# Performance work log

Hardware: AMD Instinct MI355X
Metric: run time of the kernel (lower is better)

The kernel has to match this reference:

```python
import jax, jax.numpy as jnp
import numpy as np

D_MODEL = 1024
H = 16
D_HEAD = 64  # d_q = d_k = d_v
B = 2
S = 2048


def setup_inputs() -> dict:
    key = jax.random.key(0)
    ks = jax.random.split(key, 12)
    scale = 1.0 / np.sqrt(D_MODEL)
    inp = {
        "q": jax.random.normal(ks[0], (B, S, D_MODEL), dtype=jnp.float32),
        "k": jax.random.normal(ks[1], (B, S, D_MODEL), dtype=jnp.float32),
        "v": jax.random.normal(ks[2], (B, S, D_MODEL), dtype=jnp.float32),
        "mask": jax.random.uniform(ks[3], (S, S), dtype=jnp.float32),
        # stacked per-head projection weights: [H, d_model, d_head]
        "W_q": jax.random.normal(ks[4], (H, D_MODEL, D_HEAD), dtype=jnp.float32) * scale,
        "b_q": jnp.zeros((H, D_HEAD), dtype=jnp.float32),
        "W_k": jax.random.normal(ks[5], (H, D_MODEL, D_HEAD), dtype=jnp.float32) * scale,
        "b_k": jnp.zeros((H, D_HEAD), dtype=jnp.float32),
        "W_v": jax.random.normal(ks[6], (H, D_MODEL, D_HEAD), dtype=jnp.float32) * scale,
        "b_v": jnp.zeros((H, D_HEAD), dtype=jnp.float32),
        # output projection: [H*d_v, d_model]
        "W_o": jax.random.normal(ks[7], (H * D_HEAD, D_MODEL), dtype=jnp.float32) * (1.0 / np.sqrt(H * D_HEAD)),
        "b_o": jnp.zeros((D_MODEL,), dtype=jnp.float32),
    }
    return inp


def reference(q, k, v, mask, W_q, b_q, W_k, b_k, W_v, b_v, W_o, b_o):
    # Batched QKV projections over all heads (original loops per head).
    Q = jnp.einsum("bsd,hde->bhse", q, W_q) + b_q[None, :, None, :]  # [B,H,S,Dh]
    K = jnp.einsum("bsd,hde->bhse", k, W_k) + b_k[None, :, None, :]
    V = jnp.einsum("bsd,hde->bhse", v, W_v) + b_v[None, :, None, :]
    scale = 1.0 / jnp.sqrt(jnp.asarray(D_HEAD, dtype=Q.dtype))
    # NOTE: mask is MULTIPLICATIVE on the scaled scores (as in the original).
    scores = jnp.einsum("bhse,bhte->bhst", Q, K) * scale * mask  # [B,H,S,S]
    attn = jax.nn.softmax(scores, axis=-1)
    heads = jnp.einsum("bhst,bhte->bhse", attn, V)  # [B,H,S,Dh]
    # concat heads along feature dim (head order matches torch cat order)
    concat = jnp.transpose(heads, (0, 2, 1, 3)).reshape(B, S, H * D_HEAD)
    return concat @ W_o + b_o
```

## Files before the change

kernel.cpp:

```cpp
#include <hip/hip_runtime.h>
#include <stdint.h>

#define DM 1024
#define HNUM 16
#define DH 64
#define BB 2
#define SSEQ 2048

typedef unsigned short ushort_t;
typedef __attribute__((ext_vector_type(8))) short bf16x8;
typedef __attribute__((ext_vector_type(4))) float f32x4;
typedef __attribute__((ext_vector_type(16))) float f32x16;

#define SCALE2 0.18033688011112042f
#define DEFER_THR 11.0f

__device__ __forceinline__ ushort_t f2bf(float f) {
  unsigned u = __builtin_bit_cast(unsigned, f);
  u += 0x7FFFu + ((u >> 16) & 1u);
  return (ushort_t)(u >> 16);
}
__device__ __forceinline__ float bf2f(ushort_t h) {
  return __builtin_bit_cast(float, (unsigned)h << 16);
}
__device__ __forceinline__ float fast_exp2(float x) {
#if __has_builtin(__builtin_amdgcn_exp2f)
  return __builtin_amdgcn_exp2f(x);
#else
  return exp2f(x);
#endif
}
__device__ __forceinline__ unsigned cvt_pk_bf16(float lo, float hi) {
  unsigned r;
  asm("v_cvt_pk_bf16_f32 %0, %1, %2" : "=v"(r) : "v"(lo), "v"(hi));
  return r;
}
__device__ __forceinline__ void plane32_swap(unsigned& a, unsigned& b, int hh) {
#if __has_builtin(__builtin_amdgcn_permlane32_swap)
  typedef int v2i __attribute__((ext_vector_type(2)));
  v2i r = __builtin_amdgcn_permlane32_swap((int)a, (int)b, 0, 0);
  a = (unsigned)r.x; b = (unsigned)r.y;
#else
  unsigned sa = (unsigned)__shfl_xor((int)a, 32);
  unsigned sb = (unsigned)__shfl_xor((int)b, 32);
  unsigned na = hh ? sb : a;
  unsigned nb = hh ? b : sa;
  a = na; b = nb;
#endif
}

typedef const __attribute__((address_space(1))) unsigned int* gas_ptr;
typedef __attribute__((address_space(3))) unsigned int* las_ptr;
__device__ __forceinline__ void gload_lds16(const void* g, void* l) {
  __builtin_amdgcn_global_load_lds((gas_ptr)(uintptr_t)g, (las_ptr)(uintptr_t)l, 16, 0, 0);
}

__global__ void prep_all(const float* __restrict__ q, const float* __restrict__ k,
                         const float* __restrict__ v, const float* __restrict__ mask,
                         const float* __restrict__ Wq, const float* __restrict__ Wk,
                         const float* __restrict__ Wv, const float* __restrict__ Wo,
                         ushort_t* __restrict__ qd, ushort_t* __restrict__ kd,
                         ushort_t* __restrict__ vd, ushort_t* __restrict__ maskd,
                         ushort_t* __restrict__ dq, ushort_t* __restrict__ dk,
                         ushort_t* __restrict__ dv, ushort_t* __restrict__ dWo) {
  __shared__ ushort_t T[64][65];
  const int bx = blockIdx.x, tid = threadIdx.x;
  if (bx < 6144) {
    const int z = bx >> 11, bi = bx & 2047;
    const float* src = z == 0 ? q : (z == 1 ? k : v);
    ushort_t* dst    = z == 0 ? qd : (z == 1 ? kd : vd);
    const int idx = bi * 256 + tid;
    const float4* s4 = (const float4*)src;
    float4 a = s4[idx * 2], c = s4[idx * 2 + 1];
    union { ushort_t h[8]; uint4 u; } o;
    o.h[0] = f2bf(a.x); o.h[1] = f2bf(a.y); o.h[2] = f2bf(a.z); o.h[3] = f2bf(a.w);
    o.h[4] = f2bf(c.x); o.h[5] = f2bf(c.y); o.h[6] = f2bf(c.z); o.h[7] = f2bf(c.w);
    ((uint4*)dst)[idx] = o.u;
  } else if (bx < 8192) {
    const int TG = bx - 6144;
    const int Tt = TG >> 6, G = TG & 63;
    #pragma unroll
    for (int i = 0; i < 2; ++i) {
      const int wd = tid * 2 + i;
      const int l = wd & 63, g2 = (wd >> 6) & 3, a = wd >> 8;
      const int qr = G * 32 + (l & 31);
      const int t = Tt * 64 + a * 32 + g2 * 8 + (l >> 5) * 4;
      float4 mv = *(const float4*)(mask + (size_t)qr * 2048 + t);
      union { ushort_t h4[4]; uint2 u; } pk;
      pk.h4[0] = f2bf(mv.x * SCALE2); pk.h4[1] = f2bf(mv.y * SCALE2);
      pk.h4[2] = f2bf(mv.z * SCALE2); pk.h4[3] = f2bf(mv.w * SCALE2);
      *(uint2*)(maskd + (size_t)TG * 2048 + (size_t)wd * 4) = pk.u;
    }
  } else if (bx < 8960) {
    const int id = bx - 8192;
    const int zz = id >> 4, yy = id & 15;
    const int mat = zz >> 4, g = zz & 15;
    const float* src = (mat == 0 ? Wq : (mat == 1 ? Wk : Wv)) + (size_t)g * 1024 * 64;
    ushort_t* dst    = (mat == 0 ? dq : (mat == 1 ? dk : dv)) + (size_t)g * 1024 * 64;
    const int r0 = yy * 64;
    #pragma unroll
    for (int i = 0; i < 16; ++i) {
      int idx = i * 256 + tid;
      int r = idx >> 6, c = idx & 63;
      T[r][c] = f2bf(src[(size_t)(r0 + r) * 64 + c]);
    }
    __syncthreads();
    #pragma unroll
    for (int i = 0; i < 16; ++i) {
      int idx = i * 256 + tid;
      int cc = idx >> 6, rr = idx & 63;
      dst[(size_t)cc * 1024 + r0 + rr] = T[rr][cc];
    }
  } else {
    const int id = bx - 8960;
    const int c0 = (id & 15) * 64, r0 = (id >> 4) * 64;
    #pragma unroll
    for (int i = 0; i < 16; ++i) {
      int idx = i * 256 + tid;
      int r = idx >> 6, c = idx & 63;
      T[r][c] = f2bf(Wo[(size_t)(r0 + r) * 1024 + c0 + c]);
    }
    __syncthreads();
    #pragma unroll
    for (int i = 0; i < 16; ++i) {
      int idx = i * 256 + tid;
      int cc = idx >> 6, rr = idx & 63;
      dWo[(size_t)(c0 + cc) * 1024 + r0 + rr] = T[rr][cc];
    }
  }
}

__device__ __forceinline__ void gemm_mainloop_128(const ushort_t* __restrict__ A,
                                                  const ushort_t* __restrict__ Bm,
                                                  f32x4 (&acc)[4][4], int m0, int n0, int l, int w) {
  __shared__ ushort_t As[128 * 64];
  __shared__ ushort_t Bs[128 * 64];
  const int wr = w >> 1, wc = w & 1;
  for (int ks = 0; ks < 16; ++ks) {
    const int k0 = ks * 64;
    #pragma unroll
    for (int it = 0; it < 4; ++it) {
      const int chunk = it * 4 + w;
      const int row = chunk * 8 + (l >> 3);
      const int kc = ((l & 7) * 8) ^ ((row & 7) * 8);
      gload_lds16(A + (size_t)(m0 + row) * 1024 + k0 + kc, (char*)As + chunk * 1024);
      gload_lds16(Bm + (size_t)(n0 + row) * 1024 + k0 + kc, (char*)Bs + chunk * 1024);
    }
    __syncthreads();
    #pragma unroll
    for (int kk = 0; kk < 2; ++kk) {
      bf16x8 af[4], bfr[4];
      #pragma unroll
      for (int mi = 0; mi < 4; ++mi) {
        const int row = wr * 64 + mi * 16 + (l & 15);
        const int kc = (kk * 32 + (l >> 4) * 8) ^ ((row & 7) * 8);
        af[mi] = *(const bf16x8*)(As + row * 64 + kc);
      }
      #pragma unroll
      for (int ni = 0; ni < 4; ++ni) {
        const int row = wc * 64 + ni * 16 + (l & 15);
        const int kc = (kk * 32 + (l >> 4) * 8) ^ ((row & 7) * 8);
        bfr[ni] = *(const bf16x8*)(Bs + row * 64 + kc);
      }
      #pragma unroll
      for (int mi = 0; mi < 4; ++mi)
        #pragma unroll
        for (int ni = 0; ni < 4; ++ni)
          acc[mi][ni] = __builtin_amdgcn_mfma_f32_16x16x32_bf16(af[mi], bfr[ni], acc[mi][ni], 0, 0, 0);
    }
    __syncthreads();
  }
}

__global__ __launch_bounds__(256, 2) void qkv_gemm(
    const ushort_t* __restrict__ qb, const ushort_t* __restrict__ kb, const ushort_t* __restrict__ vb,
    const ushort_t* __restrict__ Wtq, const ushort_t* __restrict__ Wtk, const ushort_t* __restrict__ Wtv,
    const float* __restrict__ bq, const float* __restrict__ bk, const float* __restrict__ bv,
    ushort_t* __restrict__ Qo, ushort_t* __restrict__ Ko, ushort_t* __restrict__ Vto) {
  const int z = blockIdx.z;
  const ushort_t* A  = z == 0 ? qb : (z == 1 ? kb : vb);
  const ushort_t* Bm = z == 0 ? Wtq : (z == 1 ? Wtk : Wtv);
  const float* bias  = z == 0 ? bq : (z == 1 ? bk : bv);
  ushort_t* out      = z == 0 ? Qo : (z == 1 ? Ko : Vto);
  const int m0 = blockIdx.x * 128, n0 = blockIdx.y * 128;
  const int tid = threadIdx.x, l = tid & 63, w = tid >> 6;
  f32x4 acc[4][4] = {};
  gemm_mainloop_128(A, Bm, acc, m0, n0, l, w);
  const int wr = w >> 1, wc = w & 1;
  #pragma unroll
  for (int mi = 0; mi < 4; ++mi) {
    #pragma unroll
    for (int ni = 0; ni < 4; ++ni) {
      const int n = n0 + wc * 64 + ni * 16 + (l & 15);
      const float bb = bias[n];
      const int mbase = m0 + wr * 64 + mi * 16 + ((l >> 4) << 2);
      if (z < 2) {
        #pragma unroll
        for (int i = 0; i < 4; ++i) {
          const int m = mbase + i;
          const size_t o = (((size_t)((m >> 11) * 16 + (n >> 6))) * 2048 + (m & 2047)) * 64 + (n & 63);
          out[o] = f2bf(acc[mi][ni][i] + bb);
        }
      } else {
        union { ushort_t h[4]; uint2 u2; } pk;
        #pragma unroll
        for (int i = 0; i < 4; ++i) pk.h[i] = f2bf(acc[mi][ni][i] + bb);
        const size_t o = (((size_t)((mbase >> 11) * 16 + (n >> 6))) * 64 + (n & 63)) * 2048 + (mbase & 2047);
        *(uint2*)(out + o) = pk.u2;
      }
    }
  }
}

__global__ __launch_bounds__(256, 2) void out_gemm(const ushort_t* __restrict__ A,
                                                   const ushort_t* __restrict__ Bm,
                                                   const float* __restrict__ bias,
                                                   float* __restrict__ out) {
  __shared__ ushort_t As[64 * 64];
  __shared__ ushort_t Bs[128 * 64];
  const int m0 = blockIdx.x * 64, n0 = blockIdx.y * 128;
  const int tid = threadIdx.x, l = tid & 63, w = tid >> 6;
  const int wr = w >> 1, wc = w & 1;
  f32x4 acc[2][4] = {};
  for (int ks = 0; ks < 16; ++ks) {
    const int k0 = ks * 64;
    #pragma unroll
    for (int it = 0; it < 6; ++it) {
      const int chunk = it * 4 + w;
      if (chunk < 8) {
        const int row = chunk * 8 + (l >> 3);
        const int kc = ((l & 7) * 8) ^ ((row & 7) * 8);
        gload_lds16(A + (size_t)(m0 + row) * 1024 + k0 + kc, (char*)As + chunk * 1024);
      } else {
        const int c2 = chunk - 8;
        const int row = c2 * 8 + (l >> 3);
        const int kc = ((l & 7) * 8) ^ ((row & 7) * 8);
        gload_lds16(Bm + (size_t)(n0 + row) * 1024 + k0 + kc, (char*)Bs + c2 * 1024);
      }
    }
    __syncthreads();
    #pragma unroll
    for (int kk = 0; kk < 2; ++kk) {
      bf16x8 af[2], bfr[4];
      #pragma unroll
      for (int mi = 0; mi < 2; ++mi) {
        const int row = wr * 32 + mi * 16 + (l & 15);
        const int kc = (kk * 32 + (l >> 4) * 8) ^ ((row & 7) * 8);
        af[mi] = *(const bf16x8*)(As + row * 64 + kc);
      }
      #pragma unroll
      for (int ni = 0; ni < 4; ++ni) {
        const int row = wc * 64 + ni * 16 + (l & 15);
        const int kc = (kk * 32 + (l >> 4) * 8) ^ ((row & 7) * 8);
        bfr[ni] = *(const bf16x8*)(Bs + row * 64 + kc);
      }
      #pragma unroll
      for (int mi = 0; mi < 2; ++mi)
        #pragma unroll
        for (int ni = 0; ni < 4; ++ni)
          acc[mi][ni] = __builtin_amdgcn_mfma_f32_16x16x32_bf16(af[mi], bfr[ni], acc[mi][ni], 0, 0, 0);
    }
    __syncthreads();
  }
  #pragma unroll
  for (int mi = 0; mi < 2; ++mi) {
    #pragma unroll
    for (int ni = 0; ni < 4; ++ni) {
      const int n = n0 + wc * 64 + ni * 16 + (l & 15);
      const float bb = bias[n];
      const int mbase = m0 + wr * 32 + mi * 16 + ((l >> 4) << 2);
      #pragma unroll
      for (int i = 0; i < 4; ++i)
        out[(size_t)(mbase + i) * 1024 + n] = acc[mi][ni][i] + bb;
    }
  }
}

__device__ __forceinline__ void stage_kv(const ushort_t* __restrict__ Kb, const ushort_t* __restrict__ Vb,
                                         int t0, ushort_t* ks, ushort_t* vs, int l, int w) {
  #pragma unroll
  for (int half = 0; half < 2; ++half) {
    const int c = half * 4 + w;
    const int r1 = c * 8 + (l >> 3);
    const int cc = ((l & 7) * 8) ^ ((r1 & 7) * 8);
    gload_lds16(Kb + (size_t)(t0 + r1) * 64 + cc, (char*)ks + c * 1024);
    gload_lds16(Vb + (size_t)r1 * 2048 + t0 + cc, (char*)vs + c * 1024);
  }
}

__global__ __launch_bounds__(256, 4) void flash_attn(const ushort_t* __restrict__ Q,
                                                     const ushort_t* __restrict__ K,
                                                     const ushort_t* __restrict__ Vt,
                                                     const ushort_t* __restrict__ maskF,
                                                     ushort_t* __restrict__ part0,
                                                     ushort_t* __restrict__ part1,
                                                     float2* __restrict__ mlp) {
  const int bh = blockIdx.y, b = bh >> 4, h = bh & 15;
  const int h2 = blockIdx.z;
  const int tid = threadIdx.x, l = tid & 63, w = tid >> 6;
  const int hh = l >> 5, q_l = l & 31;
  __shared__ ushort_t Ks[2][64 * 64];
  __shared__ ushort_t Vs[2][64 * 64];
  const ushort_t* Qb = Q + (size_t)bh * 2048 * 64;
  const ushort_t* Kb = K + (size_t)bh * 2048 * 64;
  const ushort_t* Vb = Vt + (size_t)bh * 64 * 2048;
  const int qbase = blockIdx.x * 128 + w * 32;
  const int G = qbase >> 5;
  const int tbase = h2 * 1024;

  bf16x8 qf[4];
  #pragma unroll
  for (int s = 0; s < 4; ++s)
    qf[s] = *(const bf16x8*)(Qb + (size_t)(qbase + q_l) * 64 + s * 16 + hh * 8);

  float m_run = -1e30f, l_run = 0.f;
  f32x16 po[2] = {};

  stage_kv(Kb, Vb, tbase, Ks[0], Vs[0], l, w);
  int cur = 0;

  for (int tt = 0; tt < 16; ++tt) {
    const int t0 = tbase + tt * 64;
    __syncthreads();
    if (tt + 1 < 16) stage_kv(Kb, Vb, t0 + 64, Ks[cur ^ 1], Vs[cur ^ 1], l, w);

    const ushort_t* mbase = maskF + (size_t)((t0 >> 6) * 64 + G) * 2048;
    uint2 mw[2][4];
    #pragma unroll
    for (int a = 0; a < 2; ++a)
      #pragma unroll
      for (int g2 = 0; g2 < 4; ++g2)
        mw[a][g2] = *(const uint2*)(mbase + (size_t)(((a * 4 + g2) * 64) + l) * 4);

    f32x16 sc[2] = {};
    #pragma unroll
    for (int s = 0; s < 4; ++s) {
      #pragma unroll
      for (int mt = 0; mt < 2; ++mt) {
        const int row = mt * 32 + q_l;
        const int col = (s * 16 + hh * 8) ^ ((q_l & 7) * 8);
        const bf16x8 kf = *(const bf16x8*)(Ks[cur] + row * 64 + col);
        sc[mt] = __builtin_amdgcn_mfma_f32_32x32x16_bf16(kf, qf[s], sc[mt], 0, 0, 0);
      }
    }

    float tmax = -1e30f;
    #pragma unroll
    for (int a = 0; a < 2; ++a) {
      #pragma unroll
      for (int g2 = 0; g2 < 4; ++g2) {
        const unsigned lo = mw[a][g2].x, hi = mw[a][g2].y;
        float v0 = sc[a][g2 * 4 + 0] * bf2f((ushort_t)lo);
        float v1 = sc[a][g2 * 4 + 1] * bf2f((ushort_t)(lo >> 16));
        float v2 = sc[a][g2 * 4 + 2] * bf2f((ushort_t)hi);
        float v3 = sc[a][g2 * 4 + 3] * bf2f((ushort_t)(hi >> 16));
        sc[a][g2 * 4 + 0] = v0; sc[a][g2 * 4 + 1] = v1;
        sc[a][g2 * 4 + 2] = v2; sc[a][g2 * 4 + 3] = v3;
        tmax = fmaxf(tmax, fmaxf(fmaxf(v0, v1), fmaxf(v2, v3)));
      }
    }
    tmax = fmaxf(tmax, __shfl_xor(tmax, 32));

    if (!__all(tmax <= m_run + DEFER_THR)) {
      const float mnew = fmaxf(m_run, tmax);
      const float rf = fast_exp2(m_run - mnew);
      m_run = mnew;
      l_run *= rf;
      #pragma unroll
      for (int et = 0; et < 2; ++et)
        #pragma unroll
        for (int r = 0; r < 16; ++r) po[et][r] *= rf;
    }

    float psum = 0.f;
    unsigned pw[2][8];
    #pragma unroll
    for (int a = 0; a < 2; ++a)
      #pragma unroll
      for (int j = 0; j < 8; ++j) {
        const float p0 = fast_exp2(sc[a][2 * j] - m_run);
        const float p1 = fast_exp2(sc[a][2 * j + 1] - m_run);
        psum += p0 + p1;
        pw[a][j] = cvt_pk_bf16(p0, p1);
      }
    psum += __shfl_xor(psum, 32);
    l_run += psum;

    #pragma unroll
    for (int a = 0; a < 2; ++a) {
      plane32_swap(pw[a][0], pw[a][2], hh);
      plane32_swap(pw[a][1], pw[a][3], hh);
      plane32_swap(pw[a][4], pw[a][6], hh);
      plane32_swap(pw[a][5], pw[a][7], hh);
    }

    #pragma unroll
    for (int s = 0; s < 4; ++s) {
      union { unsigned u[4]; bf16x8 v; } pf;
      pf.u[0] = pw[s >> 1][(s & 1) * 4 + 0];
      pf.u[1] = pw[s >> 1][(s & 1) * 4 + 1];
      pf.u[2] = pw[s >> 1][(s & 1) * 4 + 2];
      pf.u[3] = pw[s >> 1][(s & 1) * 4 + 3];
      #pragma unroll
      for (int et = 0; et < 2; ++et) {
        const int row = et * 32 + q_l;
        const int col = (s * 16 + hh * 8) ^ ((q_l & 7) * 8);
        const bf16x8 vf = *(const bf16x8*)(Vs[cur] + row * 64 + col);
        po[et] = __builtin_amdgcn_mfma_f32_32x32x16_bf16(vf, pf.v, po[et], 0, 0, 0);
      }
    }
    cur ^= 1;
  }

  if (hh == 0)
    mlp[(size_t)(h2 * 32 + bh) * 2048 + qbase + q_l] = make_float2(m_run, l_run);

  ushort_t* outp = h2 ? part1 : part0;
  const float invl = 1.0f / l_run;
  __syncthreads();
  ushort_t* ow = &Ks[0][0] + w * 2048;
  #pragma unroll
  for (int et = 0; et < 2; ++et)
    #pragma unroll
    for (int r = 0; r < 16; ++r) {
      const int e = et * 32 + (r & 3) + 8 * (r >> 2) + 4 * hh;
      const int ba = (q_l * 128 + e * 2) ^ ((q_l & 7) << 4);
      *(ushort_t*)((char*)ow + ba) = f2bf(po[et][r] * invl);
    }
  __syncthreads();
  {
    union { ushort_t hs[32]; uint2 u2[8]; uint4 u4[4]; } ov;
    const int ebase = hh * 32;
    #pragma unroll
    for (int c = 0; c < 8; ++c) {
      const int e0 = ebase + c * 4;
      const int ba = (q_l * 128 + e0 * 2) ^ ((q_l & 7) << 4);
      ov.u2[c] = *(const uint2*)((const char*)ow + ba);
    }
    ushort_t* dst = outp + ((size_t)(b * 2048 + qbase + q_l)) * 1024 + h * 64 + ebase;
    #pragma unroll
    for (int c2 = 0; c2 < 4; ++c2)
      ((uint4*)dst)[c2] = ov.u4[c2];
  }
}

__global__ void combine(const ushort_t* __restrict__ p0, const ushort_t* __restrict__ p1,
                        const float2* __restrict__ mlp, ushort_t* __restrict__ outc) {
  const int idx = blockIdx.x * 256 + threadIdx.x;
  const int flat = idx * 8;
  const int row = flat >> 10, col = flat & 1023;
  const int b = row >> 11, s = row & 2047, h = col >> 6;
  const int bh = b * 16 + h;
  const float2 a = mlp[(size_t)bh * 2048 + s];
  const float2 c = mlp[(size_t)(32 + bh) * 2048 + s];
  const float M = fmaxf(a.x, c.x);
  float w1 = fast_exp2(a.x - M) * a.y;
  float w2 = fast_exp2(c.x - M) * c.y;
  const float inv = 1.0f / (w1 + w2);
  w1 *= inv; w2 *= inv;
  union { uint4 u; ushort_t h8[8]; } u0, u1, o;
  u0.u = ((const uint4*)p0)[idx];
  u1.u = ((const uint4*)p1)[idx];
  #pragma unroll
  for (int j = 0; j < 8; ++j)
    o.h8[j] = f2bf(w1 * bf2f(u0.h8[j]) + w2 * bf2f(u1.h8[j]));
  ((uint4*)outc)[idx] = o.u;
}

extern "C" void kernel_launch(void* const* d_in, const int* in_sizes, int n_in,
                              void* d_out, int out_size, void* d_ws, size_t ws_size,
                              hipStream_t stream) {
  const float* q    = (const float*)d_in[0];
  const float* k    = (const float*)d_in[1];
  const float* v    = (const float*)d_in[2];
  const float* mask = (const float*)d_in[3];
  const float* Wq   = (const float*)d_in[4];
  const float* bq   = (const float*)d_in[5];
  const float* Wk   = (const float*)d_in[6];
  const float* bk   = (const float*)d_in[7];
  const float* Wv   = (const float*)d_in[8];
  const float* bv   = (const float*)d_in[9];
  const float* Wo   = (const float*)d_in[10];
  const float* bo   = (const float*)d_in[11];

  const size_t SZ8M = (size_t)4096 * 1024 * 2;
  const size_t SZ2M = (size_t)1024 * 1024 * 2;
  if (ws_size < 7 * SZ8M + 4 * SZ2M) return;

  char* p = (char*)d_ws;
  ushort_t* qb    = (ushort_t*)p; p += SZ8M;
  ushort_t* kb    = (ushort_t*)p; p += SZ8M;
  ushort_t* vb    = (ushort_t*)p; p += SZ8M;
  ushort_t* maskb = (ushort_t*)p; p += SZ8M;
  ushort_t* Qo    = (ushort_t*)p; p += SZ8M;
  ushort_t* Ko    = (ushort_t*)p; p += SZ8M;
  ushort_t* Vto   = (ushort_t*)p; p += SZ8M;
  ushort_t* Wtq   = (ushort_t*)p; p += SZ2M;
  ushort_t* Wtk   = (ushort_t*)p; p += SZ2M;
  ushort_t* Wtv   = (ushort_t*)p; p += SZ2M;
  ushort_t* Wot   = (ushort_t*)p; p += SZ2M;
  ushort_t* concat = qb;
  ushort_t* part0 = kb;
  ushort_t* part1 = vb;
  float2*   mlbuf = (float2*)Wtq;

  prep_all<<<dim3(9216), dim3(256), 0, stream>>>(q, k, v, mask, Wq, Wk, Wv, Wo,
                                                 qb, kb, vb, maskb, Wtq, Wtk, Wtv, Wot);
  qkv_gemm<<<dim3(32, 8, 3), dim3(256), 0, stream>>>(qb, kb, vb, Wtq, Wtk, Wtv, bq, bk, bv, Qo, Ko, Vto);
  flash_attn<<<dim3(16, 32, 2), dim3(256), 0, stream>>>(Qo, Ko, Vto, maskb, part0, part1, mlbuf);
  combine<<<dim3(2048), dim3(256), 0, stream>>>(part0, part1, mlbuf, concat);
  out_gemm<<<dim3(64, 8), dim3(256), 0, stream>>>(concat, Wot, bo, (float*)d_out);
}
```

Measured before the change: 138.0 us.

## Fuse split-KV partial combine into output projection GEMM A-tile load

Removes the separate combine kernel and instead merges the two split-KV attention partials inside out_gemm while staging the A tile. Each block first computes per-row, per-head softmax merge weights into shared memory, then loads both partials, blends them, converts to bf16 and writes the result to LDS. This saves one launch and the write and re-read of the concat buffer. In exchange the A-tile load becomes a synchronous register path instead of an async global-to-LDS load, and every one of the 8 column blocks redoes the combine work, so global reads of the partials grow.

```diff
diff --git a/kernel.cpp b/kernel.cpp
--- a/kernel.cpp
+++ b/kernel.cpp
@@ -212,31 +212,60 @@
   }
 }
 
-__global__ __launch_bounds__(256, 2) void out_gemm(const ushort_t* __restrict__ A,
+__global__ __launch_bounds__(256, 2) void out_gemm(const ushort_t* __restrict__ p0,
+                                                   const ushort_t* __restrict__ p1,
+                                                   const float2* __restrict__ mlp,
                                                    const ushort_t* __restrict__ Bm,
                                                    const float* __restrict__ bias,
                                                    float* __restrict__ out) {
   __shared__ ushort_t As[64 * 64];
   __shared__ ushort_t Bs[128 * 64];
+  __shared__ float Wt[2][16][64];
   const int m0 = blockIdx.x * 64, n0 = blockIdx.y * 128;
   const int tid = threadIdx.x, l = tid & 63, w = tid >> 6;
   const int wr = w >> 1, wc = w & 1;
+
+  #pragma unroll
+  for (int i = 0; i < 4; ++i) {
+    const int e = tid * 4 + i;
+    const int h = e >> 6, r = e & 63;
+    const int m = m0 + r;
+    const int b = m >> 11, s = m & 2047;
+    const int bh = b * 16 + h;
+    const float2 a = mlp[(size_t)bh * 2048 + s];
+    const float2 c = mlp[(size_t)(32 + bh) * 2048 + s];
+    const float M = fmaxf(a.x, c.x);
+    float w1 = fast_exp2(a.x - M) * a.y;
+    float w2 = fast_exp2(c.x - M) * c.y;
+    const float inv = 1.0f / (w1 + w2);
+    Wt[0][h][r] = w1 * inv;
+    Wt[1][h][r] = w2 * inv;
+  }
+  __syncthreads();
+
   f32x4 acc[2][4] = {};
   for (int ks = 0; ks < 16; ++ks) {
     const int k0 = ks * 64;
     #pragma unroll
-    for (int it = 0; it < 6; ++it) {
+    for (int it = 0; it < 4; ++it) {
+      const int c2 = it * 4 + w;
+      const int row = c2 * 8 + (l >> 3);
+      const int kc = ((l & 7) * 8) ^ ((row & 7) * 8);
+      gload_lds16(Bm + (size_t)(n0 + row) * 1024 + k0 + kc, (char*)Bs + c2 * 1024);
+    }
+    #pragma unroll
+    for (int it = 0; it < 2; ++it) {
       const int chunk = it * 4 + w;
-      if (chunk < 8) {
-        const int row = chunk * 8 + (l >> 3);
-        const int kc = ((l & 7) * 8) ^ ((row & 7) * 8);
-        gload_lds16(A + (size_t)(m0 + row) * 1024 + k0 + kc, (char*)As + chunk * 1024);
-      } else {
-        const int c2 = chunk - 8;
-        const int row = c2 * 8 + (l >> 3);
-        const int kc = ((l & 7) * 8) ^ ((row & 7) * 8);
-        gload_lds16(Bm + (size_t)(n0 + row) * 1024 + k0 + kc, (char*)Bs + c2 * 1024);
-      }
+      const int row = chunk * 8 + (l >> 3);
+      const int kc = ((l & 7) * 8) ^ ((row & 7) * 8);
+      union { uint4 u; ushort_t h8[8]; } ua, ub, oc;
+      ua.u = *(const uint4*)(p0 + (size_t)(m0 + row) * 1024 + k0 + kc);
+      ub.u = *(const uint4*)(p1 + (size_t)(m0 + row) * 1024 + k0 + kc);
+      const float w1 = Wt[0][ks][row], w2 = Wt[1][ks][row];
+      #pragma unroll
+      for (int j = 0; j < 8; ++j)
+        oc.h8[j] = f2bf(fmaf(w1, bf2f(ua.h8[j]), w2 * bf2f(ub.h8[j])));
+      *(uint4*)((char*)As + chunk * 1024 + l * 16) = oc.u;
     }
     __syncthreads();
     #pragma unroll
@@ -444,29 +473,6 @@
   }
 }
 
-__global__ void combine(const ushort_t* __restrict__ p0, const ushort_t* __restrict__ p1,
-                        const float2* __restrict__ mlp, ushort_t* __restrict__ outc) {
-  const int idx = blockIdx.x * 256 + threadIdx.x;
-  const int flat = idx * 8;
-  const int row = flat >> 10, col = flat & 1023;
-  const int b = row >> 11, s = row & 2047, h = col >> 6;
-  const int bh = b * 16 + h;
-  const float2 a = mlp[(size_t)bh * 2048 + s];
-  const float2 c = mlp[(size_t)(32 + bh) * 2048 + s];
-  const float M = fmaxf(a.x, c.x);
-  float w1 = fast_exp2(a.x - M) * a.y;
-  float w2 = fast_exp2(c.x - M) * c.y;
-  const float inv = 1.0f / (w1 + w2);
-  w1 *= inv; w2 *= inv;
-  union { uint4 u; ushort_t h8[8]; } u0, u1, o;
-  u0.u = ((const uint4*)p0)[idx];
-  u1.u = ((const uint4*)p1)[idx];
-  #pragma unroll
-  for (int j = 0; j < 8; ++j)
-    o.h8[j] = f2bf(w1 * bf2f(u0.h8[j]) + w2 * bf2f(u1.h8[j]));
-  ((uint4*)outc)[idx] = o.u;
-}
-
 extern "C" void kernel_launch(void* const* d_in, const int* in_sizes, int n_in,
                               void* d_out, int out_size, void* d_ws, size_t ws_size,
                               hipStream_t stream) {
@@ -499,7 +505,6 @@
   ushort_t* Wtk   = (ushort_t*)p; p += SZ2M;
   ushort_t* Wtv   = (ushort_t*)p; p += SZ2M;
   ushort_t* Wot   = (ushort_t*)p; p += SZ2M;
-  ushort_t* concat = qb;
   ushort_t* part0 = kb;
   ushort_t* part1 = vb;
   float2*   mlbuf = (float2*)Wtq;
@@ -508,6 +513,5 @@
                                                  qb, kb, vb, maskb, Wtq, Wtk, Wtv, Wot);
   qkv_gemm<<<dim3(32, 8, 3), dim3(256), 0, stream>>>(qb, kb, vb, Wtq, Wtk, Wtv, bq, bk, bv, Qo, Ko, Vto);
   flash_attn<<<dim3(16, 32, 2), dim3(256), 0, stream>>>(Qo, Ko, Vto, maskb, part0, part1, mlbuf);
-  combine<<<dim3(2048), dim3(256), 0, stream>>>(part0, part1, mlbuf, concat);
-  out_gemm<<<dim3(64, 8), dim3(256), 0, stream>>>(concat, Wot, bo, (float*)d_out);
-}
+  out_gemm<<<dim3(64, 8), dim3(256), 0, stream>>>(part0, part1, mlbuf, Wot, bo, (float*)d_out);
+}
```

Result: no change. 140.6 us (+1.9%).
